# Performance work log

Hardware: AMD Instinct MI355X
Metric: run time of the kernel (lower is better)

The kernel has to match this reference:

```python
import jax, jax.numpy as jnp
import numpy as np
from jax import lax

B, S, I, H = 64, 512, 1024, 1024


def _lstm_dir(x, W_ih, W_hh, b_ih, b_hh):
    # x: [B, S, I] -> hidden states [B, S, H]
    # Precompute input projections for all timesteps in one GEMM.
    xg = jnp.einsum('bsi,gi->bsg', x, W_ih) + b_ih + b_hh  # [B, S, 4H]
    Whh_T = W_hh.T  # [H, 4H]
    h0 = jnp.zeros((x.shape[0], W_hh.shape[1]), dtype=x.dtype)
    c0 = jnp.zeros_like(h0)

    def step(carry, xg_t):
        h, c = carry
        g = xg_t + h @ Whh_T  # [B, 4H]
        i_g, f_g, g_g, o_g = jnp.split(g, 4, axis=-1)  # PyTorch gate order i,f,g,o
        i_g = jax.nn.sigmoid(i_g)
        f_g = jax.nn.sigmoid(f_g)
        g_g = jnp.tanh(g_g)
        o_g = jax.nn.sigmoid(o_g)
        c = f_g * c + i_g * g_g
        h = o_g * jnp.tanh(c)
        return (h, c), h

    _, hs = lax.scan(step, (h0, c0), jnp.swapaxes(xg, 0, 1))  # hs: [S, B, H]
    return jnp.swapaxes(hs, 0, 1)


def setup_inputs() -> dict:
    key = jax.random.key(0)
    ks = jax.random.split(key, 10)
    s = 1.0 / np.sqrt(H)  # PyTorch LSTMCell init scale
    return {
        'forward_x': jax.random.normal(ks[0], (B, S, I), jnp.float32),
        'backward_x': jax.random.normal(ks[1], (B, S, I), jnp.float32),
        'W_ih_f': jax.random.uniform(ks[2], (4 * H, I), jnp.float32, -s, s),
        'W_hh_f': jax.random.uniform(ks[3], (4 * H, H), jnp.float32, -s, s),
        'b_ih_f': jax.random.uniform(ks[4], (4 * H,), jnp.float32, -s, s),
        'b_hh_f': jax.random.uniform(ks[5], (4 * H,), jnp.float32, -s, s),
        'W_ih_b': jax.random.uniform(ks[6], (4 * H, I), jnp.float32, -s, s),
        'W_hh_b': jax.random.uniform(ks[7], (4 * H, H), jnp.float32, -s, s),
        'b_ih_b': jax.random.uniform(ks[8], (4 * H,), jnp.float32, -s, s),
        'b_hh_b': jax.random.uniform(ks[9], (4 * H,), jnp.float32, -s, s),
    }


def reference(forward_x, backward_x, W_ih_f, W_hh_f, b_ih_f, b_hh_f,
              W_ih_b, W_hh_b, b_ih_b, b_hh_b):
    fwd = _lstm_dir(forward_x, W_ih_f, W_hh_f, b_ih_f, b_hh_f)
    # Backward direction consumes backward_x from the last timestep to the
    # first and writes hidden states back at their original positions,
    # i.e. run on the time-reversed sequence and reverse the outputs.
    bwd = _lstm_dir(backward_x[:, ::-1, :], W_ih_b, W_hh_b, b_ih_b, b_hh_b)[:, ::-1, :]
    return fwd, bwd
```

## Files before the change

kernel.cpp:

```cpp
#include <hip/hip_runtime.h>
#include <hip/hip_bf16.h>
#include <cstdint>


typedef __bf16 bf16_t;
typedef bf16_t bf16x8 __attribute__((ext_vector_type(8)));
typedef float  f32x4  __attribute__((ext_vector_type(4)));

#define DEVI __device__ __forceinline__

constexpr int Bb = 64, Ss = 512, Ii = 1024, Hh = 1024;
constexpr int NBLK_DIR = 128;
constexpr size_t WS_CNT    = 0;
constexpr size_t WS_HRING  = 4096;
constexpr size_t WS_XBF    = 1ull << 20;
constexpr size_t XBF_BYTES = 2ull * Ss * Bb * Ii * 2;
constexpr size_t WS_NEED_XBF = WS_XBF + XBF_BYTES;
constexpr int LDS_TOTAL = 163840;

DEVI float fast_sig(float x) {
  float z = __expf(-fabsf(x));
  float r = __builtin_amdgcn_rcpf(1.f + z);
  return x >= 0.f ? r : z * r;
}
DEVI float fast_tanh(float x) {
  float z = __expf(-2.f * fabsf(x));
  float r = (1.f - z) * __builtin_amdgcn_rcpf(1.f + z);
  return x >= 0.f ? r : -r;
}
DEVI bf16x8 cvt8(f32x4 a, f32x4 b) {
  bf16x8 r;
  r[0] = (bf16_t)a[0]; r[1] = (bf16_t)a[1]; r[2] = (bf16_t)a[2]; r[3] = (bf16_t)a[3];
  r[4] = (bf16_t)b[0]; r[5] = (bf16_t)b[1]; r[6] = (bf16_t)b[2]; r[7] = (bf16_t)b[3];
  return r;
}
DEVI f32x4 mfma16(bf16x8 a, bf16x8 b, f32x4 c) {
  return __builtin_amdgcn_mfma_f32_16x16x32_bf16(a, b, c, 0, 0, 0);
}

#define GLDS16(g, s)                                                           \
  __builtin_amdgcn_global_load_lds(                                            \
      (const __attribute__((address_space(1))) void*)(const void*)(g),         \
      (__attribute__((address_space(3))) void*)(void*)(s), 16, 0, 0)
#define GLDS16_COH(g, s)                                                       \
  __builtin_amdgcn_global_load_lds(                                            \
      (const __attribute__((address_space(1))) void*)(const void*)(g),         \
      (__attribute__((address_space(3))) void*)(void*)(s), 16, 0, 17)
#define WAIT_LGKM0 asm volatile("s_waitcnt lgkmcnt(0)" ::: "memory")
#define WAIT_VM(n) asm volatile("s_waitcnt vmcnt(" #n ")" ::: "memory")
#define BARRIER_RAW                                                            \
  do { __builtin_amdgcn_s_barrier(); __builtin_amdgcn_sched_barrier(0); } while (0)

__global__ void k_init(int* cnt) {
  int i = threadIdx.x;
  if (i < 1024) cnt[i] = 0;
}

__global__ void k_convx(const float* __restrict__ xf, const float* __restrict__ xb,
                        bf16_t* __restrict__ dst) {
  size_t og = (size_t)blockIdx.x * blockDim.x + threadIdx.x;
  int i8  = (int)(og & 127);
  int b   = (int)((og >> 7) & 63);
  int t   = (int)((og >> 13) & 511);
  int dir = (int)(og >> 22);
  const float* src = (dir ? xb : xf) + (((size_t)b * Ss + t) * Ii + (size_t)i8 * 8);
  f32x4 a = *(const f32x4*)src;
  f32x4 c = *(const f32x4*)(src + 4);
  *(bf16x8*)(dst + og * 8) = cvt8(a, c);
}

template <bool XBF>
__global__ void __launch_bounds__(512, 2)
k_lstm(const float* __restrict__ xf, const float* __restrict__ xb,
       const float* __restrict__ Wih_f, const float* __restrict__ Whh_f,
       const float* __restrict__ bih_f, const float* __restrict__ bhh_f,
       const float* __restrict__ Wih_b, const float* __restrict__ Whh_b,
       const float* __restrict__ bih_b, const float* __restrict__ bhh_b,
       float* __restrict__ out,
       const bf16_t* __restrict__ xbfin, bf16_t* __restrict__ hring,
       int* __restrict__ cnt) {
  extern __shared__ char lds[];
  char* PA = lds;
  char* PB = lds + 65536;
  float* part = (float*)(lds + 131072);

  const int tid = threadIdx.x;
  const int bid = blockIdx.x;
  const int dir = bid & 1;
  const int db  = bid >> 1;
  const int n0  = db * 8;
  const int w   = tid >> 6, l = tid & 63;
  const int u   = l >> 4, l15 = l & 15;
  const int m   = w & 1;
  const int kq  = w >> 1;

  const float* Wih = dir ? Wih_b : Wih_f;
  const float* Whh = dir ? Whh_b : Whh_f;
  const float* bih = dir ? bih_b : bih_f;
  const float* bhh = dir ? bhh_b : bhh_f;
  const float* x32 = dir ? xb : xf;
  const bf16_t* xbase = xbfin + (size_t)dir * Ss * Bb * Ii;
  bf16_t* hr = hring + (size_t)dir * 2 * Bb * Hh;
  float* outD = out + (size_t)dir * Bb * Ss * Hh;
  int* mycnt = cnt + dir * 512;

  bf16x8 wr[2][2][4][2];
#pragma unroll
  for (int mat = 0; mat < 2; ++mat)
#pragma unroll
    for (int p = 0; p < 2; ++p)
#pragma unroll
      for (int ks = 0; ks < 4; ++ks)
#pragma unroll
        for (int nt = 0; nt < 2; ++nt) {
          int c = nt * 16 + l15;
          int j = (c >> 3) * 1024 + n0 + (c & 7);
          int k = p * 512 + kq * 128 + ks * 32 + u * 8;
          const float* sp = (mat ? Whh : Wih) + (size_t)j * 1024 + k;
          wr[mat][p][ks][nt] = cvt8(*(const f32x4*)sp, *(const f32x4*)(sp + 4));
        }

  const int eb = tid >> 3, en = tid & 7;
  const int nj = n0 + en;
  float bi0 = bih[nj] + bhh[nj];
  float bi1 = bih[1024 + nj] + bhh[1024 + nj];
  float bi2 = bih[2048 + nj] + bhh[2048 + nj];
  float bi3 = bih[3072 + nj] + bhh[3072 + nj];

  int aoff0[4], aoff1[4];
#pragma unroll
  for (int ks = 0; ks < 4; ++ks) {
    int r0 = m * 32 + l15;
    int r1 = r0 + 16;
    int sl = kq * 16 + ks * 4 + u;
    aoff0[ks] = r0 * 1024 + ((sl ^ (r0 & 7)) << 4);
    aoff1[ks] = r1 * 1024 + ((sl ^ (r1 & 7)) << 4);
  }

  auto STAGE_DMA = [&](char* panel, const bf16_t* srcb) {
#pragma unroll
    for (int i = 0; i < 8; ++i) {
      const bf16_t* gp = srcb + (size_t)(w * 8 + i) * 1024 + ((l ^ i) << 3);
      char* sp = panel + (w * 8 + i) * 1024;
      GLDS16(gp, sp);
    }
  };
  auto STAGE_H = [&](char* panel, const bf16_t* srcb) {
#pragma unroll
    for (int i = 0; i < 8; ++i) {
      const bf16_t* gp = srcb + (size_t)(w * 8 + i) * 1024 + ((l ^ i) << 3);
      char* sp = panel + (w * 8 + i) * 1024;
      GLDS16_COH(gp, sp);
    }
  };
  auto STAGE_XF = [&](char* panel, const float* srcb) {
#pragma unroll
    for (int i = 0; i < 8; ++i) {
      int r = w * 8 + i;
      const float* sp = srcb + (size_t)r * (Ss * Ii) + ((l ^ i) << 3);
      f32x4 a = *(const f32x4*)sp;
      f32x4 b = *(const f32x4*)(sp + 4);
      *(bf16x8*)(panel + r * 1024 + l * 16) = cvt8(a, b);
    }
  };

  f32x4 acc00, acc01, acc10, acc11;
#define COMPUTE(panel, matC, pC)                                               \
  do {                                                                         \
    _Pragma("unroll") for (int ks = 0; ks < 4; ++ks) {                         \
      bf16x8 a0_ = *(const bf16x8*)((panel) + aoff0[ks]);                      \
      bf16x8 a1_ = *(const bf16x8*)((panel) + aoff1[ks]);                      \
      acc00 = mfma16(a0_, wr[matC][pC][ks][0], acc00);                         \
      acc01 = mfma16(a0_, wr[matC][pC][ks][1], acc01);                         \
      acc10 = mfma16(a1_, wr[matC][pC][ks][0], acc10);                         \
      acc11 = mfma16(a1_, wr[matC][pC][ks][1], acc11);                         \
    }                                                                          \
  } while (0)

  float c_reg = 0.f;

  {
    int t0 = dir ? (Ss - 1) : 0;
    if constexpr (XBF) STAGE_DMA(PA, xbase + (size_t)t0 * (Bb * Ii));
    else               STAGE_XF(PA, x32 + (size_t)t0 * Ii);
    WAIT_VM(0); WAIT_LGKM0; BARRIER_RAW;
  }

  for (int step = 0; step < Ss; ++step) {
    const int t  = dir ? (Ss - 1 - step) : step;
    const int tn = dir ? (Ss - 2 - step) : (step + 1);
    const bf16_t* hbase = hr + (size_t)((step - 1) & 1) * (Bb * Hh);

    acc00 = f32x4{0.f, 0.f, 0.f, 0.f}; acc01 = acc00; acc10 = acc00; acc11 = acc00;

    if constexpr (XBF) STAGE_DMA(PB, xbase + (size_t)t * (Bb * Ii) + 512);
    else               STAGE_XF(PB, x32 + (size_t)t * Ii + 512);
    COMPUTE(PA, 0, 0);
    WAIT_LGKM0;
    if (step > 0 && tid == 0) {
      while (__hip_atomic_load(&mycnt[step - 1], __ATOMIC_RELAXED,
                               __HIP_MEMORY_SCOPE_AGENT) < NBLK_DIR)
        __builtin_amdgcn_s_sleep(1);
    }
    BARRIER_RAW;
    if (step > 0) {
      STAGE_H(PA, hbase);
      WAIT_VM(8);
      BARRIER_RAW;
    } else {
      WAIT_VM(0); BARRIER_RAW;
    }
    COMPUTE(PB, 0, 1);
    WAIT_LGKM0; BARRIER_RAW;
    if (step > 0) {
      STAGE_H(PB, hbase + 512);
      WAIT_VM(8); BARRIER_RAW;
      COMPUTE(PA, 1, 0);
      WAIT_LGKM0; BARRIER_RAW;
    }
    if (step < Ss - 1) {
      if constexpr (XBF) STAGE_DMA(PA, xbase + (size_t)tn * (Bb * Ii));
      else               STAGE_XF(PA, x32 + (size_t)tn * Ii);
    }
    if (step > 0) {
      if (step < Ss - 1) { WAIT_VM(8); } else { WAIT_VM(0); }
      BARRIER_RAW;
      COMPUTE(PB, 1, 1);
    }
    WAIT_LGKM0; BARRIER_RAW;

#pragma unroll
    for (int rr = 0; rr < 2; ++rr)
#pragma unroll
      for (int nt = 0; nt < 2; ++nt) {
        f32x4 a = (rr == 0) ? (nt == 0 ? acc00 : acc01) : (nt == 0 ? acc10 : acc11);
#pragma unroll
        for (int q = 0; q < 4; ++q) {
          int R = m * 32 + rr * 16 + u * 4 + q;
          int C = nt * 16 + l15;
          part[(kq * 64 + R) * 32 + C] = a[q];
        }
      }
    WAIT_LGKM0; BARRIER_RAW;

    {
      float g0 = bi0, g1 = bi1, g2 = bi2, g3 = bi3;
#pragma unroll
      for (int q = 0; q < 4; ++q) {
        const float* pp = &part[(q * 64 + eb) * 32];
        g0 += pp[en]; g1 += pp[8 + en]; g2 += pp[16 + en]; g3 += pp[24 + en];
      }
      float ig = fast_sig(g0), fg = fast_sig(g1);
      float gg = fast_tanh(g2), og = fast_sig(g3);
      c_reg = fg * c_reg + ig * gg;
      float h = og * fast_tanh(c_reg);
      outD[(size_t)eb * (Ss * Hh) + (size_t)t * Hh + n0 + en] = h;
      float hn = __shfl_xor(h, 1);
      if (!(tid & 1)) {
        union { bf16_t b[2]; uint32_t u32; } pk;
        pk.b[0] = (bf16_t)h; pk.b[1] = (bf16_t)hn;
        uint32_t* dst = (uint32_t*)&hr[(size_t)(step & 1) * (Bb * Hh) +
                                       (size_t)eb * Hh + n0 + en];
        __hip_atomic_store(dst, pk.u32, __ATOMIC_RELAXED, __HIP_MEMORY_SCOPE_AGENT);
      }
    }
    WAIT_VM(0); WAIT_LGKM0; BARRIER_RAW;
    if (tid == 0) {
      __hip_atomic_fetch_add(&mycnt[step], 1, __ATOMIC_RELAXED,
                             __HIP_MEMORY_SCOPE_AGENT);
    }
  }
#undef COMPUTE
}

extern "C" void kernel_launch(void* const* d_in, const int* in_sizes, int n_in,
                              void* d_out, int out_size, void* d_ws, size_t ws_size,
                              hipStream_t stream) {
  (void)in_sizes; (void)n_in; (void)out_size;
  const float* xf    = (const float*)d_in[0];
  const float* xb    = (const float*)d_in[1];
  const float* Wih_f = (const float*)d_in[2];
  const float* Whh_f = (const float*)d_in[3];
  const float* bih_f = (const float*)d_in[4];
  const float* bhh_f = (const float*)d_in[5];
  const float* Wih_b = (const float*)d_in[6];
  const float* Whh_b = (const float*)d_in[7];
  const float* bih_b = (const float*)d_in[8];
  const float* bhh_b = (const float*)d_in[9];
  float* outp = (float*)d_out;
  char* ws = (char*)d_ws;
  int* cntp = (int*)(ws + WS_CNT);
  bf16_t* hringp = (bf16_t*)(ws + WS_HRING);
  const bf16_t* xbfp = (const bf16_t*)(ws + WS_XBF);
  const bool use_xbf = ws_size >= WS_NEED_XBF;

  hipLaunchKernelGGL(k_init, dim3(1), dim3(1024), 0, stream, cntp);
  if (use_xbf) {
    hipLaunchKernelGGL(k_convx, dim3(32768), dim3(256), 0, stream,
                       xf, xb, (bf16_t*)(ws + WS_XBF));
  }

  void* args[] = {&xf, &xb, &Wih_f, &Whh_f, &bih_f, &bhh_f,
                  &Wih_b, &Whh_b, &bih_b, &bhh_b,
                  &outp, &xbfp, &hringp, &cntp};
  if (use_xbf) {
    void (*kp)(const float*, const float*, const float*, const float*,
               const float*, const float*, const float*, const float*,
               const float*, const float*, float*, const bf16_t*, bf16_t*, int*) =
        k_lstm<true>;
    hipFuncSetAttribute((const void*)kp, hipFuncAttributeMaxDynamicSharedMemorySize,
                        LDS_TOTAL);
    hipLaunchCooperativeKernel((const void*)kp, dim3(256), dim3(512), args,
                               LDS_TOTAL, stream);
  } else {
    void (*kp)(const float*, const float*, const float*, const float*,
               const float*, const float*, const float*, const float*,
               const float*, const float*, float*, const bf16_t*, bf16_t*, int*) =
        k_lstm<false>;
    hipFuncSetAttribute((const void*)kp, hipFuncAttributeMaxDynamicSharedMemorySize,
                        LDS_TOTAL);
    hipLaunchCooperativeKernel((const void*)kp, dim3(256), dim3(512), args,
                               LDS_TOTAL, stream);
  }
}
```

Before: 3.565 ms.

## Replace atomic step counter with per-block flags and swizzle partial-sum LDS

Cross-block step synchronisation changes from a per-step counter incremented by atomic fetch_add (polled by one thread with sleep) to one flag per block, written with a plain atomic store. 128 threads each poll one flag in a tight loop with no sleep. This is meant to remove contention on a single atomic address and the latency of the sleep-based poll on the serial recurrence path, at the cost of more polling traffic. The partial-sum LDS buffer also gets an XOR swizzle on its column index to reduce bank conflicts in the reduction.

```diff
diff --git a/kernel.cpp b/kernel.cpp
--- a/kernel.cpp
+++ b/kernel.cpp
@@ -10,8 +10,7 @@
 #define DEVI __device__ __forceinline__
 
 constexpr int Bb = 64, Ss = 512, Ii = 1024, Hh = 1024;
-constexpr int NBLK_DIR = 128;
-constexpr size_t WS_CNT    = 0;
+constexpr size_t WS_FLAGS  = 0;
 constexpr size_t WS_HRING  = 4096;
 constexpr size_t WS_XBF    = 1ull << 20;
 constexpr size_t XBF_BYTES = 2ull * Ss * Bb * Ii * 2;
@@ -51,9 +50,9 @@
 #define BARRIER_RAW                                                            \
   do { __builtin_amdgcn_s_barrier(); __builtin_amdgcn_sched_barrier(0); } while (0)
 
-__global__ void k_init(int* cnt) {
+__global__ void k_init(int* flags) {
   int i = threadIdx.x;
-  if (i < 1024) cnt[i] = 0;
+  if (i < 256) flags[i] = 0;
 }
 
 __global__ void k_convx(const float* __restrict__ xf, const float* __restrict__ xb,
@@ -78,7 +77,7 @@
        const float* __restrict__ bih_b, const float* __restrict__ bhh_b,
        float* __restrict__ out,
        const bf16_t* __restrict__ xbfin, bf16_t* __restrict__ hring,
-       int* __restrict__ cnt) {
+       int* __restrict__ flags) {
   extern __shared__ char lds[];
   char* PA = lds;
   char* PB = lds + 65536;
@@ -102,7 +101,7 @@
   const bf16_t* xbase = xbfin + (size_t)dir * Ss * Bb * Ii;
   bf16_t* hr = hring + (size_t)dir * 2 * Bb * Hh;
   float* outD = out + (size_t)dir * Bb * Ss * Hh;
-  int* mycnt = cnt + dir * 512;
+  int* myflags = flags + dir * 128;
 
   bf16x8 wr[2][2][4][2];
 #pragma unroll
@@ -197,10 +196,10 @@
     else               STAGE_XF(PB, x32 + (size_t)t * Ii + 512);
     COMPUTE(PA, 0, 0);
     WAIT_LGKM0;
-    if (step > 0 && tid == 0) {
-      while (__hip_atomic_load(&mycnt[step - 1], __ATOMIC_RELAXED,
-                               __HIP_MEMORY_SCOPE_AGENT) < NBLK_DIR)
-        __builtin_amdgcn_s_sleep(1);
+    if (step > 0 && tid < 128) {
+      const int* fp = &myflags[tid];
+      while (__hip_atomic_load(fp, __ATOMIC_RELAXED, __HIP_MEMORY_SCOPE_AGENT) < step) {
+      }
     }
     BARRIER_RAW;
     if (step > 0) {
@@ -238,17 +237,19 @@
         for (int q = 0; q < 4; ++q) {
           int R = m * 32 + rr * 16 + u * 4 + q;
           int C = nt * 16 + l15;
-          part[(kq * 64 + R) * 32 + C] = a[q];
+          part[(kq * 64 + R) * 32 + (C ^ ((R & 7) << 2))] = a[q];
         }
       }
     WAIT_LGKM0; BARRIER_RAW;
 
     {
+      const int sk = (eb & 7) << 2;
       float g0 = bi0, g1 = bi1, g2 = bi2, g3 = bi3;
 #pragma unroll
       for (int q = 0; q < 4; ++q) {
         const float* pp = &part[(q * 64 + eb) * 32];
-        g0 += pp[en]; g1 += pp[8 + en]; g2 += pp[16 + en]; g3 += pp[24 + en];
+        g0 += pp[en ^ sk]; g1 += pp[(8 + en) ^ sk];
+        g2 += pp[(16 + en) ^ sk]; g3 += pp[(24 + en) ^ sk];
       }
       float ig = fast_sig(g0), fg = fast_sig(g1);
       float gg = fast_tanh(g2), og = fast_sig(g3);
@@ -266,8 +267,8 @@
     }
     WAIT_VM(0); WAIT_LGKM0; BARRIER_RAW;
     if (tid == 0) {
-      __hip_atomic_fetch_add(&mycnt[step], 1, __ATOMIC_RELAXED,
-                             __HIP_MEMORY_SCOPE_AGENT);
+      __hip_atomic_store(&myflags[db], step + 1, __ATOMIC_RELAXED,
+                         __HIP_MEMORY_SCOPE_AGENT);
     }
   }
 #undef COMPUTE
@@ -289,12 +290,12 @@
   const float* bhh_b = (const float*)d_in[9];
   float* outp = (float*)d_out;
   char* ws = (char*)d_ws;
-  int* cntp = (int*)(ws + WS_CNT);
+  int* flagsp = (int*)(ws + WS_FLAGS);
   bf16_t* hringp = (bf16_t*)(ws + WS_HRING);
   const bf16_t* xbfp = (const bf16_t*)(ws + WS_XBF);
   const bool use_xbf = ws_size >= WS_NEED_XBF;
 
-  hipLaunchKernelGGL(k_init, dim3(1), dim3(1024), 0, stream, cntp);
+  hipLaunchKernelGGL(k_init, dim3(1), dim3(256), 0, stream, flagsp);
   if (use_xbf) {
     hipLaunchKernelGGL(k_convx, dim3(32768), dim3(256), 0, stream,
                        xf, xb, (bf16_t*)(ws + WS_XBF));
@@ -302,7 +303,7 @@
 
   void* args[] = {&xf, &xb, &Wih_f, &Whh_f, &bih_f, &bhh_f,
                   &Wih_b, &Whh_b, &bih_b, &bhh_b,
-                  &outp, &xbfp, &hringp, &cntp};
+                  &outp, &xbfp, &hringp, &flagsp};
   if (use_xbf) {
     void (*kp)(const float*, const float*, const float*, const float*,
                const float*, const float*, const float*, const float*,
```

After: 3.439 ms. 3.5% less time.
